# Kernel optimization log

Measured on AMD Instinct MI355X. Metric: run time of the kernel, lower is better.

## Reference

```python
import jax, jax.numpy as jnp
import numpy as np

DIM = 1024
HEADS = 16


def setup_inputs() -> dict:
    key = jax.random.key(0)
    k1, k2, k3, k4 = jax.random.split(key, 4)
    X = jax.random.normal(k1, (4, 2048, DIM), dtype=jnp.float32)
    # torch Linear weight is [out, in]; store transposed [in, out] for x @ W
    W_qkv = jax.random.normal(k2, (DIM, 3 * DIM), dtype=jnp.float32) * (DIM ** -0.5)
    W_out = jax.random.normal(k3, (DIM, DIM), dtype=jnp.float32) * (DIM ** -0.5)
    b_out = jax.random.normal(k4, (DIM,), dtype=jnp.float32) * 0.01
    return {"X": X, "W_qkv": W_qkv, "W_out": W_out, "b_out": b_out}


def reference(X, W_qkv, W_out, b_out):
    b, t, d = X.shape
    h = HEADS
    hd = d // h
    scale = d ** -0.5  # NOTE: scales by full dim, matching the original module
    qkv = X @ W_qkv  # [b, t, 3d]
    q, k, v = jnp.split(qkv, 3, axis=-1)
    # [b, t, d] -> [b, h, t, hd]
    def to_heads(x):
        return x.reshape(b, t, h, hd).transpose(0, 2, 1, 3)
    q, k, v = to_heads(q), to_heads(k), to_heads(v)
    dots = jnp.einsum('bhid,bhjd->bhij', q, k) * scale  # [b, h, t, t]
    attn = jax.nn.softmax(dots, axis=-1)
    out = jnp.einsum('bhij,bhjd->bhid', attn, v)  # [b, h, t, hd]
    out = out.transpose(0, 2, 1, 3).reshape(b, t, d)
    return out @ W_out + b_out
```

## Files before the change

### kernel.cpp

```cpp
#include <hip/hip_runtime.h>
#include <hip/hip_bf16.h>
#include <stdint.h>

#define DIMD 1024
#define NB 4
#define NT 2048
#define NH 16
#define BT (NB*NT)
#define NQKV (3*DIMD)

typedef __attribute__((ext_vector_type(8))) __bf16 bf16x8;
typedef __attribute__((ext_vector_type(4))) __bf16 bf16x4;
typedef __attribute__((ext_vector_type(4))) float f32x4;
typedef __attribute__((ext_vector_type(16))) float f32x16;

#define MFMA16(a,b,c) __builtin_amdgcn_mfma_f32_16x16x32_bf16((a),(b),(c),0,0,0)
#define MFMA32(a,b,c) __builtin_amdgcn_mfma_f32_32x32x16_bf16((a),(b),(c),0,0,0)

#define QSCALE 0.0450842200277801f

__device__ __forceinline__ void gld16(const void* g, void* l) {
  __builtin_amdgcn_global_load_lds((const __attribute__((address_space(1))) void*)g,
                                   (__attribute__((address_space(3))) void*)l,
                                   16, 0, 0);
}

__device__ __forceinline__ unsigned pkbf(float a, float b) {
  unsigned short ua = __builtin_bit_cast(unsigned short, (__bf16)a);
  unsigned short ub = __builtin_bit_cast(unsigned short, (__bf16)b);
  return (unsigned)ua | ((unsigned)ub << 16);
}

__global__ __launch_bounds__(256) void k_cvt(const float* __restrict__ in,
                                             __bf16* __restrict__ out, int n4) {
  int i = blockIdx.x * blockDim.x + threadIdx.x;
  int st = gridDim.x * blockDim.x;
  for (; i < n4; i += st) {
    float4 v = ((const float4*)in)[i];
    bf16x4 o;
    o[0] = (__bf16)v.x; o[1] = (__bf16)v.y; o[2] = (__bf16)v.z; o[3] = (__bf16)v.w;
    ((bf16x4*)out)[i] = o;
  }
}

__global__ __launch_bounds__(256) void k_tcvt(const float* __restrict__ in,
                                              __bf16* __restrict__ out, int K, int N) {
  __shared__ __bf16 t[64][72];
  int n0 = blockIdx.x * 64, k0 = blockIdx.y * 64;
  int r = threadIdx.x >> 2, c0 = (threadIdx.x & 3) * 16;
  const float4* src = (const float4*)(in + (size_t)(k0 + r) * N + n0 + c0);
#pragma unroll
  for (int i = 0; i < 4; ++i) {
    float4 v = src[i];
    t[r][c0 + i*4 + 0] = (__bf16)v.x;
    t[r][c0 + i*4 + 1] = (__bf16)v.y;
    t[r][c0 + i*4 + 2] = (__bf16)v.z;
    t[r][c0 + i*4 + 3] = (__bf16)v.w;
  }
  __syncthreads();
  bf16x8 o0, o1;
#pragma unroll
  for (int i = 0; i < 8; ++i) o0[i] = t[c0 + i][r];
#pragma unroll
  for (int i = 0; i < 8; ++i) o1[i] = t[c0 + 8 + i][r];
  __bf16* dst = out + (size_t)(n0 + r) * K + k0 + c0;
  *(bf16x8*)dst = o0;
  *(bf16x8*)(dst + 8) = o1;
}

template<int MODE>
__global__ __launch_bounds__(256) void k_gemm(const __bf16* __restrict__ A,
                                              const __bf16* __restrict__ Bt,
                                              int M, int N, int K,
                                              __bf16* __restrict__ oQK,
                                              __bf16* __restrict__ oVt,
                                              float* __restrict__ oF,
                                              const float* __restrict__ bias) {
  __shared__ alignas(16) __bf16 As[128 * 32];
  __shared__ alignas(16) __bf16 Bs[128 * 32];
  const int tid = threadIdx.x;
  const int lane = tid & 63, w = tid >> 6;
  const int lr = lane & 15, lo = lane >> 4;
  const int wm = w >> 1, wn = w & 1;
  const int m0 = blockIdx.y * 128, n0 = blockIdx.x * 128;
  const __bf16* Ab = A + (size_t)m0 * K;
  const __bf16* Bb = Bt + (size_t)n0 * K;
  f32x4 acc[4][4] = {};
  const int s0i = tid, s1i = 256 + tid;

  for (int k0 = 0; k0 < K; k0 += 32) {
    gld16(Ab + (size_t)(s0i >> 2) * K + k0 + (s0i & 3) * 8, (char*)As + s0i * 16);
    gld16(Ab + (size_t)(s1i >> 2) * K + k0 + (s1i & 3) * 8, (char*)As + s1i * 16);
    gld16(Bb + (size_t)(s0i >> 2) * K + k0 + (s0i & 3) * 8, (char*)Bs + s0i * 16);
    gld16(Bb + (size_t)(s1i >> 2) * K + k0 + (s1i & 3) * 8, (char*)Bs + s1i * 16);
    asm volatile("s_waitcnt vmcnt(0)" ::: "memory");
    __syncthreads();
    bf16x8 af[4], bfr[4];
#pragma unroll
    for (int mt = 0; mt < 4; ++mt)
      af[mt] = *(const bf16x8*)(As + (wm*64 + mt*16 + lr) * 32 + lo * 8);
#pragma unroll
    for (int nt = 0; nt < 4; ++nt)
      bfr[nt] = *(const bf16x8*)(Bs + (wn*64 + nt*16 + lr) * 32 + lo * 8);
#pragma unroll
    for (int mt = 0; mt < 4; ++mt)
#pragma unroll
      for (int nt = 0; nt < 4; ++nt)
        acc[mt][nt] = MFMA16(af[mt], bfr[nt], acc[mt][nt]);
    __syncthreads();
  }

  if (MODE == 0) {
    const int cb = n0 + wn * 64;
    if (cb < 2048) {
      const float f = (cb < 1024) ? QSCALE : 1.0f;
#pragma unroll
      for (int mt = 0; mt < 4; ++mt)
#pragma unroll
        for (int nt = 0; nt < 4; ++nt) {
          int col = cb + nt * 16 + lr;
          int mrow = m0 + wm * 64 + mt * 16 + lo * 4;
#pragma unroll
          for (int r = 0; r < 4; ++r)
            oQK[(size_t)(mrow + r) * 2048 + col] = (__bf16)(acc[mt][nt][r] * f);
        }
    } else {
#pragma unroll
      for (int mt = 0; mt < 4; ++mt)
#pragma unroll
        for (int nt = 0; nt < 4; ++nt) {
          int dd = cb - 2048 + nt * 16 + lr;
          int mrow = m0 + wm * 64 + mt * 16 + lo * 4;
          int bb = mrow >> 11, tt = mrow & 2047;
          bf16x4 pk;
#pragma unroll
          for (int r = 0; r < 4; ++r) pk[r] = (__bf16)acc[mt][nt][r];
          *(bf16x4*)(oVt + ((size_t)(bb << 10) + dd) * 2048 + tt) = pk;
        }
    }
  } else {
#pragma unroll
    for (int mt = 0; mt < 4; ++mt)
#pragma unroll
      for (int nt = 0; nt < 4; ++nt) {
        int col = n0 + wn * 64 + nt * 16 + lr;
        float bv = bias[col];
        int mrow = m0 + wm * 64 + mt * 16 + lo * 4;
#pragma unroll
        for (int r = 0; r < 4; ++r)
          oF[(size_t)(mrow + r) * N + col] = acc[mt][nt][r] + bv;
      }
  }
}

__global__ __launch_bounds__(256, 2) void k_attn(const __bf16* __restrict__ QK,
                                                 const __bf16* __restrict__ Vt,
                                                 __bf16* __restrict__ AO) {
  __shared__ alignas(16) __bf16 Ks[2][64 * 72];
  __shared__ alignas(16) __bf16 Vs[2][64 * 72];
  const int tid = threadIdx.x, w = tid >> 6, lane = tid & 63;
  const int l31 = lane & 31, hi = lane >> 5;
  const int P = blockIdx.x;
  const int low3 = P & 7, g = P >> 3;
  const int qc = g & 7;
  const int bh = ((g >> 3) << 3) + low3;
  const int h = bh & 15, b = bh >> 4;
  const int q0 = qc * 256 + w * 64;

  bf16x8 qfA[4], qfB[4];
  {
    const __bf16* Qb = QK + (size_t)(b * 2048 + q0 + l31) * 2048 + h * 64 + hi * 8;
#pragma unroll
    for (int dc = 0; dc < 4; ++dc) qfA[dc] = *(const bf16x8*)(Qb + dc * 16);
    Qb += (size_t)32 * 2048;
#pragma unroll
    for (int dc = 0; dc < 4; ++dc) qfB[dc] = *(const bf16x8*)(Qb + dc * 16);
  }
  const __bf16* Kg = QK + (size_t)(b * 2048) * 2048 + 1024 + h * 64;
  const __bf16* Vg = Vt + (size_t)(b * 1024 + h * 64) * 2048;

  const int i0 = tid, i1 = 256 + tid, i2 = 512 + tid;
  int r0 = i0 / 9, c0 = i0 - r0 * 9; c0 = (c0 == 8) ? 0 : c0;
  int r1 = i1 / 9, c1 = i1 - r1 * 9; c1 = (c1 == 8) ? 0 : c1;
  int r2 = i2 / 9, c2 = i2 - r2 * 9; c2 = (c2 == 8) ? 0 : c2;
  const __bf16* kP0 = Kg + (size_t)r0 * 2048 + c0 * 8;
  const __bf16* kP1 = Kg + (size_t)r1 * 2048 + c1 * 8;
  const __bf16* kP2 = Kg + (size_t)r2 * 2048 + c2 * 8;
  const __bf16* vP0 = Vg + (size_t)r0 * 2048 + c0 * 8;
  const __bf16* vP1 = Vg + (size_t)r1 * 2048 + c1 * 8;
  const __bf16* vP2 = Vg + (size_t)r2 * 2048 + c2 * 8;

  f32x16 oA0 = {0,0,0,0,0,0,0,0,0,0,0,0,0,0,0,0};
  f32x16 oA1 = {0,0,0,0,0,0,0,0,0,0,0,0,0,0,0,0};
  f32x16 oB0 = {0,0,0,0,0,0,0,0,0,0,0,0,0,0,0,0};
  f32x16 oB1 = {0,0,0,0,0,0,0,0,0,0,0,0,0,0,0,0};
  float lnA = 0.f, lnB = 0.f;

  auto STAGE = [&](int x) {
    char* bK = (char*)&Ks[x][0];
    char* bV = (char*)&Vs[x][0];
    gld16(kP0, bK + i0 * 16);
    gld16(vP0, bV + i0 * 16);
    gld16(kP1, bK + i1 * 16);
    gld16(vP1, bV + i1 * 16);
    if (tid < 64) {
      gld16(kP2, bK + i2 * 16);
      gld16(vP2, bV + i2 * 16);
    }
    kP0 += 64 * 2048; kP1 += 64 * 2048; kP2 += 64 * 2048;
    vP0 += 64; vP1 += 64; vP2 += 64;
  };

  auto SMPACK = [&](const f32x16& s0, const f32x16& s1, unsigned pw[4][4], float& ln) {
    float p0a[16], p1a[16];
#pragma unroll
    for (int r = 0; r < 16; ++r) {
      p0a[r] = __builtin_amdgcn_exp2f(s0[r]);
      p1a[r] = __builtin_amdgcn_exp2f(s1[r]);
    }
    float sA = 0.f, sB = 0.f, sC = 0.f, sD = 0.f;
#pragma unroll
    for (int r = 0; r < 4; ++r) {
      sA += p0a[r];      sB += p0a[4 + r];
      sC += p0a[8 + r];  sD += p0a[12 + r];
      sA += p1a[r];      sB += p1a[4 + r];
      sC += p1a[8 + r];  sD += p1a[12 + r];
    }
    ln += (sA + sB) + (sC + sD);
#pragma unroll
    for (int c = 0; c < 4; ++c) {
      const float* pp = (c < 2) ? p0a : p1a;
      const int rb = (c & 1) * 8;
      unsigned A01 = pkbf(pp[rb + 0], pp[rb + 1]);
      unsigned A23 = pkbf(pp[rb + 2], pp[rb + 3]);
      unsigned A45 = pkbf(pp[rb + 4], pp[rb + 5]);
      unsigned A67 = pkbf(pp[rb + 6], pp[rb + 7]);
      asm("v_permlane32_swap_b32 %0, %1" : "+v"(A01), "+v"(A45));
      asm("v_permlane32_swap_b32 %0, %1" : "+v"(A23), "+v"(A67));
      pw[c][0] = A01; pw[c][1] = A23; pw[c][2] = A45; pw[c][3] = A67;
    }
  };

  STAGE(0);
  asm volatile("s_waitcnt vmcnt(0)" ::: "memory");
  __syncthreads();

  int x = 0;
#pragma unroll 2
  for (int t = 0; t < 32; ++t) {
    if (t < 31) STAGE(x ^ 1);
    const __bf16* Kl = &Ks[x][0];
    const __bf16* Vl = &Vs[x][0];

    f32x16 sA0 = {0,0,0,0,0,0,0,0,0,0,0,0,0,0,0,0};
    f32x16 sA1 = {0,0,0,0,0,0,0,0,0,0,0,0,0,0,0,0};
    f32x16 sB0 = {0,0,0,0,0,0,0,0,0,0,0,0,0,0,0,0};
    f32x16 sB1 = {0,0,0,0,0,0,0,0,0,0,0,0,0,0,0,0};
    {
      bf16x8 kf[8];
#pragma unroll
      for (int dc = 0; dc < 4; ++dc)
        kf[dc] = *(const bf16x8*)(Kl + l31 * 72 + dc * 16 + hi * 8);
#pragma unroll
      for (int dc = 0; dc < 4; ++dc)
        kf[4 + dc] = *(const bf16x8*)(Kl + (32 + l31) * 72 + dc * 16 + hi * 8);
      __builtin_amdgcn_s_setprio(1);
#pragma unroll
      for (int dc = 0; dc < 4; ++dc) {
        sA0 = MFMA32(kf[dc], qfA[dc], sA0);
        sB0 = MFMA32(kf[dc], qfB[dc], sB0);
        sA1 = MFMA32(kf[4 + dc], qfA[dc], sA1);
        sB1 = MFMA32(kf[4 + dc], qfB[dc], sB1);
      }
      __builtin_amdgcn_s_setprio(0);
    }

    unsigned pwA[4][4], pwB[4][4];
    SMPACK(sA0, sA1, pwA, lnA);
    SMPACK(sB0, sB1, pwB, lnB);

    {
      bf16x8 vf[8];
#pragma unroll
      for (int c = 0; c < 4; ++c)
        vf[c] = *(const bf16x8*)(Vl + l31 * 72 + c * 16 + hi * 8);
#pragma unroll
      for (int c = 0; c < 4; ++c)
        vf[4 + c] = *(const bf16x8*)(Vl + (32 + l31) * 72 + c * 16 + hi * 8);
      __builtin_amdgcn_s_setprio(1);
#pragma unroll
      for (int c = 0; c < 4; ++c) {
        union { unsigned u[4]; bf16x8 v; } pa, pb;
        pa.u[0] = pwA[c][0]; pa.u[1] = pwA[c][1]; pa.u[2] = pwA[c][2]; pa.u[3] = pwA[c][3];
        pb.u[0] = pwB[c][0]; pb.u[1] = pwB[c][1]; pb.u[2] = pwB[c][2]; pb.u[3] = pwB[c][3];
        oA0 = MFMA32(pa.v, vf[c], oA0);
        oB0 = MFMA32(pb.v, vf[c], oB0);
        oA1 = MFMA32(pa.v, vf[4 + c], oA1);
        oB1 = MFMA32(pb.v, vf[4 + c], oB1);
      }
      __builtin_amdgcn_s_setprio(0);
    }

    asm volatile("s_waitcnt vmcnt(0)" ::: "memory");
    __syncthreads();
    x ^= 1;
  }

  float lA = lnA + __shfl_xor(lnA, 32, 64);
  float lB = lnB + __shfl_xor(lnB, 32, 64);
  float invA = 1.0f / lA, invB = 1.0f / lB;
  __bf16* Ob = AO + (size_t)(b * 2048 + q0) * 1024 + h * 64;
#pragma unroll
  for (int r = 0; r < 16; ++r) {
    int qr = (r & 3) + 8 * (r >> 2) + 4 * hi;
    float ivA = __shfl(invA, qr, 64);
    float ivB = __shfl(invB, qr, 64);
    Ob[(size_t)qr * 1024 + l31] = (__bf16)(oA0[r] * ivA);
    Ob[(size_t)qr * 1024 + 32 + l31] = (__bf16)(oA1[r] * ivA);
    Ob[(size_t)(32 + qr) * 1024 + l31] = (__bf16)(oB0[r] * ivB);
    Ob[(size_t)(32 + qr) * 1024 + 32 + l31] = (__bf16)(oB1[r] * ivB);
  }
}

extern "C" void kernel_launch(void* const* d_in, const int* in_sizes, int n_in,
                              void* d_out, int out_size, void* d_ws, size_t ws_size,
                              hipStream_t stream) {
  const float* X    = (const float*)d_in[0];
  const float* Wqkv = (const float*)d_in[1];
  const float* Wout = (const float*)d_in[2];
  const float* bout = (const float*)d_in[3];
  float* out = (float*)d_out;
  char* ws = (char*)d_ws;

  __bf16* Xb  = (__bf16*)(ws);
  __bf16* Wqt = (__bf16*)(ws + 16777216);
  __bf16* Wot = (__bf16*)(ws + 23068672);
  __bf16* QKb = (__bf16*)(ws + 25165824);
  __bf16* Vtb = (__bf16*)(ws + 58720256);
  __bf16* AOb = (__bf16*)(ws + 75497472);

  k_cvt<<<2048, 256, 0, stream>>>(X, Xb, (BT * DIMD) / 4);
  k_tcvt<<<dim3(NQKV / 64, DIMD / 64), 256, 0, stream>>>(Wqkv, Wqt, DIMD, NQKV);
  k_tcvt<<<dim3(DIMD / 64, DIMD / 64), 256, 0, stream>>>(Wout, Wot, DIMD, DIMD);
  k_gemm<0><<<dim3(NQKV / 128, BT / 128), 256, 0, stream>>>(
      Xb, Wqt, BT, NQKV, DIMD, QKb, Vtb, nullptr, nullptr);
  k_attn<<<512, 256, 0, stream>>>(QKb, Vtb, AOb);
  k_gemm<1><<<dim3(DIMD / 128, BT / 128), 256, 0, stream>>>(
      AOb, Wot, BT, DIMD, DIMD, nullptr, nullptr, out, bout);
}
```

Before: 207.3 us.

## Rewrite projection GEMMs with 128x256 tiles and a 4-stage async LDS pipeline

Replaces the 128x128, single-buffered GEMM with a 512-thread kernel that computes 128x256 tiles. Global-to-LDS loads run through a 4-stage ring with three tiles in flight, using partial vmcnt waits and one barrier per k-step. It also adds an XCD-aware block swizzle and raises MFMA priority during the compute phase. The aim is to hide global load latency and cut the sync overhead of the old load-wait-compute loop, at the cost of 96KB of LDS per block and one block per CU. K is hardcoded to 1024.

```diff
diff --git a/kernel.cpp b/kernel.cpp
--- a/kernel.cpp
+++ b/kernel.cpp
@@ -69,86 +69,115 @@
 }
 
 template<int MODE>
-__global__ __launch_bounds__(256) void k_gemm(const __bf16* __restrict__ A,
-                                              const __bf16* __restrict__ Bt,
-                                              int M, int N, int K,
-                                              __bf16* __restrict__ oQK,
-                                              __bf16* __restrict__ oVt,
-                                              float* __restrict__ oF,
-                                              const float* __restrict__ bias) {
-  __shared__ alignas(16) __bf16 As[128 * 32];
-  __shared__ alignas(16) __bf16 Bs[128 * 32];
+__global__ __launch_bounds__(512, 1) void k_gemm256(const __bf16* __restrict__ A,
+                                                    const __bf16* __restrict__ Bt,
+                                                    int nbx,
+                                                    __bf16* __restrict__ oQK,
+                                                    __bf16* __restrict__ oVt,
+                                                    float* __restrict__ oF,
+                                                    const float* __restrict__ bias) {
+  constexpr int KK = 1024, KT = 32;
+  __shared__ alignas(16) char L[98304];
   const int tid = threadIdx.x;
-  const int lane = tid & 63, w = tid >> 6;
+  const int lane = tid & 63, wid = tid >> 6;
   const int lr = lane & 15, lo = lane >> 4;
-  const int wm = w >> 1, wn = w & 1;
-  const int m0 = blockIdx.y * 128, n0 = blockIdx.x * 128;
-  const __bf16* Ab = A + (size_t)m0 * K;
-  const __bf16* Bb = Bt + (size_t)n0 * K;
+  const int wm = wid >> 2, wn = wid & 3;
+  const int cpx = gridDim.x >> 3;
+  const int swz = (blockIdx.x & 7) * cpx + (blockIdx.x >> 3);
+  const int bx = swz % nbx, by = swz / nbx;
+  const int m0 = by * 128, n0 = bx * 256;
+
+  const int srow = tid >> 2, sk = (tid & 3) * 8;
+  const __bf16* Asr = A + (size_t)(m0 + srow) * KK + sk;
+  const __bf16* Bs0 = Bt + (size_t)(n0 + srow) * KK + sk;
+  const __bf16* Bs1 = Bt + (size_t)(n0 + 128 + srow) * KK + sk;
+
+  auto STAGE = [&](int t) {
+    const int s = t & 3;
+    char* dA = L + s * 8192 + tid * 16;
+    char* dB = L + 32768 + s * 16384 + tid * 16;
+    gld16(Asr + t * 32, dA);
+    gld16(Bs0 + t * 32, dB);
+    gld16(Bs1 + t * 32, dB + 8192);
+  };
+
+  const __bf16* fA = (const __bf16*)L + (size_t)(wm * 64 + lr) * 32 + lo * 8;
+  const __bf16* fB = (const __bf16*)(L + 32768) + (size_t)(wn * 64 + lr) * 32 + lo * 8;
+
   f32x4 acc[4][4] = {};
-  const int s0i = tid, s1i = 256 + tid;
-
-  for (int k0 = 0; k0 < K; k0 += 32) {
-    gld16(Ab + (size_t)(s0i >> 2) * K + k0 + (s0i & 3) * 8, (char*)As + s0i * 16);
-    gld16(Ab + (size_t)(s1i >> 2) * K + k0 + (s1i & 3) * 8, (char*)As + s1i * 16);
-    gld16(Bb + (size_t)(s0i >> 2) * K + k0 + (s0i & 3) * 8, (char*)Bs + s0i * 16);
-    gld16(Bb + (size_t)(s1i >> 2) * K + k0 + (s1i & 3) * 8, (char*)Bs + s1i * 16);
-    asm volatile("s_waitcnt vmcnt(0)" ::: "memory");
-    __syncthreads();
-    bf16x8 af[4], bfr[4];
-#pragma unroll
-    for (int mt = 0; mt < 4; ++mt)
-      af[mt] = *(const bf16x8*)(As + (wm*64 + mt*16 + lr) * 32 + lo * 8);
-#pragma unroll
-    for (int nt = 0; nt < 4; ++nt)
-      bfr[nt] = *(const bf16x8*)(Bs + (wn*64 + nt*16 + lr) * 32 + lo * 8);
-#pragma unroll
-    for (int mt = 0; mt < 4; ++mt)
-#pragma unroll
-      for (int nt = 0; nt < 4; ++nt)
-        acc[mt][nt] = MFMA16(af[mt], bfr[nt], acc[mt][nt]);
-    __syncthreads();
-  }
-
+  STAGE(0); STAGE(1); STAGE(2);
+
+  for (int t = 0; t < KT; ++t) {
+    if (t < KT - 2)       asm volatile("s_waitcnt vmcnt(6)" ::: "memory");
+    else if (t == KT - 2) asm volatile("s_waitcnt vmcnt(3)" ::: "memory");
+    else                  asm volatile("s_waitcnt vmcnt(0)" ::: "memory");
+    asm volatile("s_barrier" ::: "memory");
+    if (t + 3 < KT) STAGE(t + 3);
+    const __bf16* fa = fA + (t & 3) * 4096;
+    const __bf16* fb = fB + (t & 3) * 8192;
+    bf16x8 Af[4], Bf[4];
+#pragma unroll
+    for (int i = 0; i < 4; ++i) Af[i] = *(const bf16x8*)(fa + i * 512);
+#pragma unroll
+    for (int j = 0; j < 4; ++j) Bf[j] = *(const bf16x8*)(fb + j * 512);
+    __builtin_amdgcn_s_setprio(1);
+#pragma unroll
+    for (int i = 0; i < 4; ++i)
+#pragma unroll
+      for (int j = 0; j < 4; ++j)
+        acc[i][j] = MFMA16(Af[i], Bf[j], acc[i][j]);
+    __builtin_amdgcn_s_setprio(0);
+  }
+
+  const int mb = m0 + wm * 64 + lo * 4;
   if (MODE == 0) {
-    const int cb = n0 + wn * 64;
-    if (cb < 2048) {
-      const float f = (cb < 1024) ? QSCALE : 1.0f;
-#pragma unroll
-      for (int mt = 0; mt < 4; ++mt)
-#pragma unroll
-        for (int nt = 0; nt < 4; ++nt) {
-          int col = cb + nt * 16 + lr;
-          int mrow = m0 + wm * 64 + mt * 16 + lo * 4;
+    if (n0 < 1024) {
+#pragma unroll
+      for (int i = 0; i < 4; ++i)
+#pragma unroll
+        for (int j = 0; j < 4; ++j) {
+          int col = n0 + wn * 64 + j * 16 + lr;
+          int row = mb + i * 16;
 #pragma unroll
           for (int r = 0; r < 4; ++r)
-            oQK[(size_t)(mrow + r) * 2048 + col] = (__bf16)(acc[mt][nt][r] * f);
+            oQK[(size_t)(row + r) * 2048 + col] = (__bf16)(acc[i][j][r] * QSCALE);
+        }
+    } else if (n0 < 2048) {
+#pragma unroll
+      for (int i = 0; i < 4; ++i)
+#pragma unroll
+        for (int j = 0; j < 4; ++j) {
+          int col = n0 + wn * 64 + j * 16 + lr;
+          int row = mb + i * 16;
+#pragma unroll
+          for (int r = 0; r < 4; ++r)
+            oQK[(size_t)(row + r) * 2048 + col] = (__bf16)acc[i][j][r];
         }
     } else {
 #pragma unroll
-      for (int mt = 0; mt < 4; ++mt)
-#pragma unroll
-        for (int nt = 0; nt < 4; ++nt) {
-          int dd = cb - 2048 + nt * 16 + lr;
-          int mrow = m0 + wm * 64 + mt * 16 + lo * 4;
-          int bb = mrow >> 11, tt = mrow & 2047;
+      for (int i = 0; i < 4; ++i)
+#pragma unroll
+        for (int j = 0; j < 4; ++j) {
+          int dd = n0 - 2048 + wn * 64 + j * 16 + lr;
+          int row = mb + i * 16;
+          int bb = row >> 11, tt = row & 2047;
           bf16x4 pk;
 #pragma unroll
-          for (int r = 0; r < 4; ++r) pk[r] = (__bf16)acc[mt][nt][r];
+          for (int r = 0; r < 4; ++r) pk[r] = (__bf16)acc[i][j][r];
           *(bf16x4*)(oVt + ((size_t)(bb << 10) + dd) * 2048 + tt) = pk;
         }
     }
   } else {
 #pragma unroll
-    for (int mt = 0; mt < 4; ++mt)
-#pragma unroll
-      for (int nt = 0; nt < 4; ++nt) {
-        int col = n0 + wn * 64 + nt * 16 + lr;
+    for (int i = 0; i < 4; ++i)
+#pragma unroll
+      for (int j = 0; j < 4; ++j) {
+        int col = n0 + wn * 64 + j * 16 + lr;
         float bv = bias[col];
-        int mrow = m0 + wm * 64 + mt * 16 + lo * 4;
+        int row = mb + i * 16;
 #pragma unroll
         for (int r = 0; r < 4; ++r)
-          oF[(size_t)(mrow + r) * N + col] = acc[mt][nt][r] + bv;
+          oF[(size_t)(row + r) * 1024 + col] = acc[i][j][r] + bv;
       }
   }
 }
@@ -342,9 +371,7 @@
   k_cvt<<<2048, 256, 0, stream>>>(X, Xb, (BT * DIMD) / 4);
   k_tcvt<<<dim3(NQKV / 64, DIMD / 64), 256, 0, stream>>>(Wqkv, Wqt, DIMD, NQKV);
   k_tcvt<<<dim3(DIMD / 64, DIMD / 64), 256, 0, stream>>>(Wout, Wot, DIMD, DIMD);
-  k_gemm<0><<<dim3(NQKV / 128, BT / 128), 256, 0, stream>>>(
-      Xb, Wqt, BT, NQKV, DIMD, QKb, Vtb, nullptr, nullptr);
+  k_gemm256<0><<<768, 512, 0, stream>>>(Xb, Wqt, 12, QKb, Vtb, nullptr, nullptr);
   k_attn<<<512, 256, 0, stream>>>(QKb, Vtb, AOb);
-  k_gemm<1><<<dim3(DIMD / 128, BT / 128), 256, 0, stream>>>(
-      AOb, Wot, BT, DIMD, DIMD, nullptr, nullptr, out, bout);
-}
+  k_gemm256<1><<<256, 512, 0, stream>>>(AOb, Wot, 4, nullptr, nullptr, out, bout);
+}
```

New measurement: 204.1 us. No clear change (-1.5%).
